# Kernel optimization log

Measured on AMD Instinct MI355X. Metric: run time of the kernel, lower is better.

The kernel has to match this reference:

```python
import jax, jax.numpy as jnp
import numpy as np

VOCAB = 32000
H_EMB = 128
TOTAL_SUBTOKENS = 1_000_000
N_NODES = 200_000
PAD_IDX = 0  # nn.Embedding(padding_idx=pad) keeps that row zero


def setup_inputs() -> dict:
    key = jax.random.key(0)
    k1, k2, k3 = jax.random.split(key, 3)
    table = jax.random.normal(k1, (VOCAB, H_EMB), dtype=jnp.float32)
    table = table.at[PAD_IDX].set(0.0)  # padding row is zeros
    subtoken_ids = jax.random.randint(k2, (TOTAL_SUBTOKENS,), 0, VOCAB, dtype=jnp.int64)
    # sorted segment ids emulate contiguous per-node slices of the concatenated subtoken list
    segment_ids = jnp.sort(jax.random.randint(k3, (TOTAL_SUBTOKENS,), 0, N_NODES, dtype=jnp.int64))
    return {
        "subtoken_table": table,
        "subtoken_ids": subtoken_ids,
        "segment_ids": segment_ids,
        "n_nodes": N_NODES,
    }


def reference(subtoken_table, subtoken_ids, segment_ids, n_nodes):
    # fused embedding gather + per-node ragged sum pooling
    # [total_subtokens, h_emb] gather, then segment-sum to [n_nodes, h_emb]
    subtoken_embeds = subtoken_table[subtoken_ids]
    token_embeds = jax.ops.segment_sum(
        subtoken_embeds, segment_ids, num_segments=n_nodes,
        indices_are_sorted=True,
    )
    return token_embeds
```

## Files before the change

### kernel.cpp

```cpp
#include <hip/hip_runtime.h>


#define H_EMB   128
#define SPG     8
#define UNROLL  16
#define ROW_U1  64

__device__ __forceinline__ unsigned f2bf_rne(float f) {
    unsigned u = __float_as_uint(f);
    return (u + 0x7FFFu + ((u >> 16) & 1u)) >> 16;
}

__device__ __forceinline__ void nt_store2(float* p, float x, float y) {
    unsigned long long v = (unsigned long long)__float_as_uint(x)
                         | ((unsigned long long)__float_as_uint(y) << 32);
    __builtin_nontemporal_store(v, (unsigned long long*)p);
}

__global__ __launch_bounds__(256)
void prep_kernel(const float* __restrict__ t, unsigned* __restrict__ ct, int n_pairs,
                 const int* __restrict__ segs, int* __restrict__ starts,
                 int n, int n_nodes)
{
    const int i = blockIdx.x * blockDim.x + threadIdx.x;
    if (i < n_pairs) {
        unsigned long long w =
            __builtin_nontemporal_load((const unsigned long long*)t + i);
        const float fx = __uint_as_float((unsigned)w);
        const float fy = __uint_as_float((unsigned)(w >> 32));
        ct[i] = f2bf_rne(fx) | (f2bf_rne(fy) << 16);
    }
    if (i < n) {
        const int s  = __builtin_nontemporal_load(segs + i);
        const int sp = (i == 0) ? -1 : __builtin_nontemporal_load(segs + i - 1);
        for (int seg = sp + 1; seg <= s; ++seg) starts[seg] = i;
        if (i == n - 1)
            for (int seg = s + 1; seg <= n_nodes; ++seg) starts[seg] = n;
    }
}

__global__ __launch_bounds__(256)
void SubTokenEmbedding_6734508720780_kernel(
    const unsigned* __restrict__ ctab,
    const int*      __restrict__ ids,
    const int*      __restrict__ segs,
    const int*      __restrict__ starts,
    float*          __restrict__ out,
    int n_nodes)
{
    const int wave = (int)((blockIdx.x * blockDim.x + threadIdx.x) >> 6);
    const int lane = (int)(threadIdx.x & 63);
    const int s0   = wave * SPG;
    if (s0 >= n_nodes) return;
    const int s_end = min(s0 + SPG, n_nodes);

    const int beg = starts[s0];
    const int end = starts[s_end];

    const unsigned* trow = ctab + lane;
    float*          orow = out  + lane * 2;

    float accx = 0.f, accy = 0.f;
    int cur = s0;

    int sv = 0, iv = 0;
    if (beg + lane < end) {
        sv = __builtin_nontemporal_load(segs + beg + lane);
        iv = __builtin_nontemporal_load(ids  + beg + lane);
    }

    for (int base = beg; base < end; base += 64) {
        const int cnt = min(64, end - base);
        const int nb  = base + 64;
        int sv2 = 0, iv2 = 0;
        if (nb + lane < end) {
            sv2 = __builtin_nontemporal_load(segs + nb + lane);
            iv2 = __builtin_nontemporal_load(ids  + nb + lane);
        }

        for (int k = 0; k < cnt; k += UNROLL) {
            int s_a[UNROLL], id_a[UNROLL];
            #pragma unroll
            for (int u = 0; u < UNROLL; ++u) {
                s_a[u]  = __builtin_amdgcn_readlane(sv, k + u);
                id_a[u] = __builtin_amdgcn_readlane(iv, k + u);
            }
            unsigned tv[UNROLL];
            #pragma unroll
            for (int u = 0; u < UNROLL; ++u)
                tv[u] = trow[(size_t)id_a[u] * ROW_U1];

            #pragma unroll
            for (int u = 0; u < UNROLL; ++u) {
                if (k + u < cnt) {
                    const int s = s_a[u];
                    if (s != cur) {
                        nt_store2(orow + (size_t)cur * H_EMB, accx, accy);
                        accx = 0.f; accy = 0.f;
                        for (int z = cur + 1; z < s; ++z)
                            nt_store2(orow + (size_t)z * H_EMB, 0.f, 0.f);
                        cur = s;
                    }
                    accx += __uint_as_float(tv[u] << 16);
                    accy += __uint_as_float(tv[u] & 0xFFFF0000u);
                }
            }
        }
        sv = sv2; iv = iv2;
    }

    nt_store2(orow + (size_t)cur * H_EMB, accx, accy);
    for (int z = cur + 1; z < s_end; ++z)
        nt_store2(orow + (size_t)z * H_EMB, 0.f, 0.f);
}

__global__ __launch_bounds__(256)
void subtok_f32_kernel(
    const float* __restrict__ table,
    const int*   __restrict__ ids,
    const int*   __restrict__ segs,
    float*       __restrict__ out,
    int total_subtokens, int n_nodes)
{
    const int group = (int)((blockIdx.x * blockDim.x + threadIdx.x) / 32);
    const int lane  = (int)(threadIdx.x & 31);
    const int s0    = group * SPG;
    if (s0 >= n_nodes) return;
    const int s_end = min(s0 + SPG, n_nodes);

    auto lower_bound = [&](int v) -> int {
        int lo = 0, hi = total_subtokens;
        while (lo < hi) { int m = (lo + hi) >> 1; if (segs[m] < v) lo = m + 1; else hi = m; }
        return lo;
    };
    const int beg = lower_bound(s0);
    const int end = lower_bound(s_end);

    const float* trow = table + (size_t)lane * 4;
    float*       orow = out   + (size_t)lane * 4;
    float4 acc = make_float4(0.f, 0.f, 0.f, 0.f);
    int cur = s0;

    for (int j = beg; j < end; ++j) {
        const int s  = segs[j];
        const int id = ids[j];
        if (s != cur) {
            *reinterpret_cast<float4*>(orow + (size_t)cur * H_EMB) = acc;
            const float4 zero = make_float4(0.f, 0.f, 0.f, 0.f);
            for (int z = cur + 1; z < s; ++z)
                *reinterpret_cast<float4*>(orow + (size_t)z * H_EMB) = zero;
            acc = zero; cur = s;
        }
        const float4 t = *reinterpret_cast<const float4*>(trow + (size_t)id * H_EMB);
        acc.x += t.x; acc.y += t.y; acc.z += t.z; acc.w += t.w;
    }
    *reinterpret_cast<float4*>(orow + (size_t)cur * H_EMB) = acc;
    const float4 zero = make_float4(0.f, 0.f, 0.f, 0.f);
    for (int z = cur + 1; z < s_end; ++z)
        *reinterpret_cast<float4*>(orow + (size_t)z * H_EMB) = zero;
}

extern "C" void kernel_launch(void* const* d_in, const int* in_sizes, int n_in,
                              void* d_out, int out_size, void* d_ws, size_t ws_size,
                              hipStream_t stream) {
    const float* table = (const float*)d_in[0];
    const int*   ids   = (const int*)d_in[1];
    const int*   segs  = (const int*)d_in[2];
    float*       out   = (float*)d_out;

    const int total_subtokens = in_sizes[1];
    const int vocab           = in_sizes[0] / H_EMB;
    const int n_nodes         = out_size / H_EMB;

    const size_t starts_bytes = ((size_t)(n_nodes + 1) * sizeof(int) + 15) & ~(size_t)15;
    const size_t ctab_bytes   = (size_t)vocab * (H_EMB / 2) * sizeof(unsigned);
    const int    n_pairs      = vocab * (H_EMB / 2);

    if (ws_size >= starts_bytes + ctab_bytes) {
        int*      starts = (int*)d_ws;
        unsigned* ctab   = (unsigned*)((char*)d_ws + starts_bytes);

        const int prep_n = max(n_pairs, total_subtokens);
        prep_kernel<<<(prep_n + 255) / 256, 256, 0, stream>>>(
            table, ctab, n_pairs, segs, starts, total_subtokens, n_nodes);

        const int n_waves  = (n_nodes + SPG - 1) / SPG;
        const int n_blocks = (n_waves + 3) / 4;
        SubTokenEmbedding_6734508720780_kernel<<<n_blocks, 256, 0, stream>>>(
            ctab, ids, segs, starts, out, n_nodes);
    } else {
        const int n_groups = (n_nodes + SPG - 1) / SPG;
        const int n_blocks = (n_groups + 7) / 8;
        subtok_f32_kernel<<<n_blocks, 256, 0, stream>>>(
            table, ids, segs, out, total_subtokens, n_nodes);
    }
}
```

Measured before the change: 66.43 us.

## Split bf16 table into column halves and run two half-width pooling passes

The prep kernel now writes the bf16-packed table as two separate column-half tables (64 columns each). The pooling kernel runs twice, once per half, with 32-lane groups over 64 columns. The aim is to shrink the working set each pass touches (half the table, about 4 MB) so it stays in cache, and to raise parallelism by using half-waves. The cost is reading ids and segs twice, extra per-lane shuffles in place of readlane, and a second kernel launch.

```diff
diff --git a/kernel.cpp b/kernel.cpp
--- a/kernel.cpp
+++ b/kernel.cpp
@@ -2,9 +2,10 @@
 
 
 #define H_EMB   128
+#define LPG     32
 #define SPG     8
-#define UNROLL  16
-#define ROW_U1  64
+#define UNROLL  8
+#define HROW_U  32
 
 __device__ __forceinline__ unsigned f2bf_rne(float f) {
     unsigned u = __float_as_uint(f);
@@ -18,17 +19,24 @@
 }
 
 __global__ __launch_bounds__(256)
-void prep_kernel(const float* __restrict__ t, unsigned* __restrict__ ct, int n_pairs,
+void prep_kernel(const float* __restrict__ t, unsigned* __restrict__ ctabA,
+                 int n_pairs, int vocab,
                  const int* __restrict__ segs, int* __restrict__ starts,
                  int n, int n_nodes)
 {
     const int i = blockIdx.x * blockDim.x + threadIdx.x;
     if (i < n_pairs) {
+        const int r = i >> 6;
+        const int c = i & 63;
         unsigned long long w =
             __builtin_nontemporal_load((const unsigned long long*)t + i);
         const float fx = __uint_as_float((unsigned)w);
         const float fy = __uint_as_float((unsigned)(w >> 32));
-        ct[i] = f2bf_rne(fx) | (f2bf_rne(fy) << 16);
+        const unsigned packed = f2bf_rne(fx) | (f2bf_rne(fy) << 16);
+        unsigned* dst = (c < 32)
+            ? ctabA + (size_t)r * HROW_U + c
+            : ctabA + (size_t)vocab * HROW_U + (size_t)r * HROW_U + (c - 32);
+        *dst = packed;
     }
     if (i < n) {
         const int s  = __builtin_nontemporal_load(segs + i);
@@ -41,23 +49,23 @@
 
 __global__ __launch_bounds__(256)
 void SubTokenEmbedding_6734508720780_kernel(
-    const unsigned* __restrict__ ctab,
+    const unsigned* __restrict__ ctabH,
     const int*      __restrict__ ids,
     const int*      __restrict__ segs,
     const int*      __restrict__ starts,
     float*          __restrict__ out,
     int n_nodes)
 {
-    const int wave = (int)((blockIdx.x * blockDim.x + threadIdx.x) >> 6);
-    const int lane = (int)(threadIdx.x & 63);
-    const int s0   = wave * SPG;
+    const int group = (int)((blockIdx.x * blockDim.x + threadIdx.x) / LPG);
+    const int lane  = (int)(threadIdx.x & (LPG - 1));
+    const int s0    = group * SPG;
     if (s0 >= n_nodes) return;
     const int s_end = min(s0 + SPG, n_nodes);
 
     const int beg = starts[s0];
     const int end = starts[s_end];
 
-    const unsigned* trow = ctab + lane;
+    const unsigned* trow = ctabH + lane;
     float*          orow = out  + lane * 2;
 
     float accx = 0.f, accy = 0.f;
@@ -69,9 +77,9 @@
         iv = __builtin_nontemporal_load(ids  + beg + lane);
     }
 
-    for (int base = beg; base < end; base += 64) {
-        const int cnt = min(64, end - base);
-        const int nb  = base + 64;
+    for (int base = beg; base < end; base += LPG) {
+        const int cnt = min(LPG, end - base);
+        const int nb  = base + LPG;
         int sv2 = 0, iv2 = 0;
         if (nb + lane < end) {
             sv2 = __builtin_nontemporal_load(segs + nb + lane);
@@ -82,13 +90,13 @@
             int s_a[UNROLL], id_a[UNROLL];
             #pragma unroll
             for (int u = 0; u < UNROLL; ++u) {
-                s_a[u]  = __builtin_amdgcn_readlane(sv, k + u);
-                id_a[u] = __builtin_amdgcn_readlane(iv, k + u);
+                s_a[u]  = __shfl(sv, k + u, LPG);
+                id_a[u] = __shfl(iv, k + u, LPG);
             }
             unsigned tv[UNROLL];
             #pragma unroll
             for (int u = 0; u < UNROLL; ++u)
-                tv[u] = trow[(size_t)id_a[u] * ROW_U1];
+                tv[u] = trow[(size_t)id_a[u] * HROW_U];
 
             #pragma unroll
             for (int u = 0; u < UNROLL; ++u) {
@@ -173,21 +181,26 @@
     const int n_nodes         = out_size / H_EMB;
 
     const size_t starts_bytes = ((size_t)(n_nodes + 1) * sizeof(int) + 15) & ~(size_t)15;
-    const size_t ctab_bytes   = (size_t)vocab * (H_EMB / 2) * sizeof(unsigned);
+    const size_t ctab_bytes   = 2 * (size_t)vocab * HROW_U * sizeof(unsigned);
     const int    n_pairs      = vocab * (H_EMB / 2);
 
     if (ws_size >= starts_bytes + ctab_bytes) {
         int*      starts = (int*)d_ws;
-        unsigned* ctab   = (unsigned*)((char*)d_ws + starts_bytes);
+        unsigned* ctabA  = (unsigned*)((char*)d_ws + starts_bytes);
+        unsigned* ctabB  = ctabA + (size_t)vocab * HROW_U;
 
         const int prep_n = max(n_pairs, total_subtokens);
         prep_kernel<<<(prep_n + 255) / 256, 256, 0, stream>>>(
-            table, ctab, n_pairs, segs, starts, total_subtokens, n_nodes);
-
-        const int n_waves  = (n_nodes + SPG - 1) / SPG;
-        const int n_blocks = (n_waves + 3) / 4;
+            table, ctabA, n_pairs, vocab, segs, starts, total_subtokens, n_nodes);
+
+        const int n_groups         = (n_nodes + SPG - 1) / SPG;
+        const int groups_per_block = 256 / LPG;
+        const int n_blocks         = (n_groups + groups_per_block - 1) / groups_per_block;
+
         SubTokenEmbedding_6734508720780_kernel<<<n_blocks, 256, 0, stream>>>(
-            ctab, ids, segs, starts, out, n_nodes);
+            ctabA, ids, segs, starts, out, n_nodes);
+        SubTokenEmbedding_6734508720780_kernel<<<n_blocks, 256, 0, stream>>>(
+            ctabB, ids, segs, starts, out + 64, n_nodes);
     } else {
         const int n_groups = (n_nodes + SPG - 1) / SPG;
         const int n_blocks = (n_groups + 7) / 8;
```

After: 71.47 us. 1.08x slower.
